# Performance work log

Measured on AMD Instinct MI355X. Metric: run time of the kernel, lower is better.

## Reference

```python
import jax, jax.numpy as jnp
import numpy as np

N, E = 100000, 1200000
IN_NF, H_NF, OUT_NF, IN_EF = 32, 64, 64, 16


def _linear_params(key, fan_in, fan_out):
    kw, kb = jax.random.split(key)
    s = 1.0 / np.sqrt(fan_in)
    W = jax.random.uniform(kw, (fan_in, fan_out), jnp.float32, -s, s)
    b = jax.random.uniform(kb, (fan_out,), jnp.float32, -s, s)
    return W, b


def setup_inputs() -> dict:
    key = jax.random.key(0)
    ks = jax.random.split(key, 16)
    inp = {
        'node_feats': jax.random.normal(ks[0], (N, IN_NF), jnp.float32),
        'edge_attr': jax.random.normal(ks[1], (E, IN_EF), jnp.float32),
        'coords': jax.random.normal(ks[2], (N, 3), jnp.float32),
        'edge_index': jax.random.randint(ks[3], (2, E), 0, N, jnp.int64),
    }
    # emb_in / emb_out
    inp['W_in'], inp['b_in'] = _linear_params(ks[4], IN_NF, H_NF)
    inp['W_out'], inp['b_out'] = _linear_params(ks[5], H_NF, OUT_NF)
    # edge MLP: cat[h_i, h_j, radial, edge_attr] -> hidden -> hidden
    edge_in = 2 * H_NF + 1 + IN_EF
    inp['We1'], inp['be1'] = _linear_params(ks[6], edge_in, H_NF)
    inp['We2'], inp['be2'] = _linear_params(ks[7], H_NF, H_NF)
    # node MLP: cat[h, agg_m] -> hidden -> out
    inp['Wn1'], inp['bn1'] = _linear_params(ks[8], H_NF + H_NF, H_NF)
    inp['Wn2'], inp['bn2'] = _linear_params(ks[9], H_NF, H_NF)
    # coord MLP: m -> hidden -> 1
    inp['Wc1'], inp['bc1'] = _linear_params(ks[10], H_NF, H_NF)
    inp['Wc2'], inp['bc2'] = _linear_params(ks[11], H_NF, 1)
    return inp


def _egnn_fwd(node_feats, edge_attr, coords, edge_index,
              W_in, b_in, We1, be1, We2, be2, Wn1, bn1, Wn2, bn2,
              Wc1, bc1, Wc2, bc2, W_out, b_out):
    relu = jax.nn.relu
    n = node_feats.shape[0]
    row, col = edge_index[0], edge_index[1]

    h = node_feats @ W_in + b_in                       # [N, H]

    # --- edge model ---
    coord_diff = coords[row] - coords[col]             # [E, 3]
    radial = jnp.sum(coord_diff * coord_diff, axis=-1, keepdims=True)  # [E, 1]
    edge_in = jnp.concatenate([h[row], h[col], radial, edge_attr], axis=-1)
    m = relu(relu(edge_in @ We1 + be1) @ We2 + be2)    # [E, H]

    # --- coord model: mean-aggregate coord_diff * phi_x(m) ---
    trans = coord_diff * (relu(m @ Wc1 + bc1) @ Wc2 + bc2)  # [E, 3]
    agg_x = jax.ops.segment_sum(trans, row, num_segments=n)
    cnt = jax.ops.segment_sum(jnp.ones((trans.shape[0],), trans.dtype), row, num_segments=n)
    coords = coords + agg_x / jnp.maximum(cnt, 1.0)[:, None]

    # --- node model: sum-aggregate messages ---
    agg_m = jax.ops.segment_sum(m, row, num_segments=n)  # [N, H]
    h = relu(jnp.concatenate([h, agg_m], axis=-1) @ Wn1 + bn1) @ Wn2 + bn2

    out = h @ W_out + b_out                            # [N, OUT]
    return out, coords


def reference(node_feats, edge_attr, coords, edge_index,
              W_in, b_in, W_out, b_out, We1, be1, We2, be2,
              Wn1, bn1, Wn2, bn2, Wc1, bc1, Wc2, bc2):
    return _egnn_fwd(node_feats, edge_attr, coords, edge_index,
                     W_in, b_in, We1, be1, We2, be2, Wn1, bn1, Wn2, bn2,
                     Wc1, bc1, Wc2, bc2, W_out, b_out)
```

## Files before the change

### kernel.cpp

```cpp
#include <hip/hip_runtime.h>


typedef __attribute__((ext_vector_type(4))) float f32x4;
typedef __attribute__((ext_vector_type(8))) short short8;

__device__ __forceinline__ void atomAddF(float* p, float v) { unsafeAtomicAdd(p, v); }

__device__ __forceinline__ unsigned short f2bf(float f) {
  unsigned int u = __builtin_bit_cast(unsigned int, f);
  unsigned int r = (u + 0x7FFFu + ((u >> 16) & 1u)) >> 16;
  return (unsigned short)r;
}
__device__ __forceinline__ float bf2f(unsigned short s) {
  unsigned int v = ((unsigned int)s) << 16;
  return __builtin_bit_cast(float, v);
}
__device__ __forceinline__ float lo_bf(unsigned int u) {
  return __builtin_bit_cast(float, u << 16);
}
__device__ __forceinline__ float hi_bf(unsigned int u) {
  return __builtin_bit_cast(float, u & 0xFFFF0000u);
}

__global__ __launch_bounds__(256) void k_prep(
    const float* __restrict__ nf, const float* __restrict__ W_in,
    const float* __restrict__ b_in, const float* __restrict__ We1,
    const float* __restrict__ be1, const float* __restrict__ Wn1,
    const float* __restrict__ bn1, const float* __restrict__ Wn2,
    const float* __restrict__ bn2, const float* __restrict__ W_out,
    const float* __restrict__ b_out, unsigned short* __restrict__ nfb,
    float* __restrict__ WA, float* __restrict__ WB, float* __restrict__ WF1,
    float* __restrict__ Wno, float* __restrict__ bSum, float* __restrict__ bn1f,
    float* __restrict__ bno, float* __restrict__ aggz, int N) {
  const int b = blockIdx.x, t = threadIdx.x;
  if (b == 0 || b == 1) {
    const float* Wsrc = (b == 0) ? We1 : (We1 + 64 * 64);
    float* dst = (b == 0) ? WA : WB;
    for (int idx = t; idx < 2048; idx += 256) {
      const int i = idx >> 6, n = idx & 63;
      float s = 0.f;
      for (int h = 0; h < 64; ++h) s = fmaf(W_in[i * 64 + h], Wsrc[h * 64 + n], s);
      dst[idx] = s;
    }
  } else if (b == 2) {
    for (int idx = t; idx < 2048; idx += 256) {
      const int i = idx >> 6, n = idx & 63;
      float s = 0.f;
      for (int h = 0; h < 64; ++h) s = fmaf(W_in[i * 64 + h], Wn1[h * 64 + n], s);
      WF1[idx] = s;
    }
    if (t < 64) {
      float s1 = bn1[t], s2 = be1[t];
      for (int h = 0; h < 64; ++h) {
        s1 = fmaf(b_in[h], Wn1[h * 64 + t], s1);
        s2 = fmaf(b_in[h], We1[h * 64 + t] + We1[(64 + h) * 64 + t], s2);
      }
      bn1f[t] = s1;
      bSum[t] = s2;
    }
  } else if (b <= 6) {
    const int base = (b - 3) * 1024;
    for (int idx = t; idx < 1024; idx += 256) {
      const int kk = (base + idx) >> 6, n = (base + idx) & 63;
      float s = 0.f;
      for (int h = 0; h < 64; ++h) s = fmaf(Wn2[kk * 64 + h], W_out[h * 64 + n], s);
      Wno[base + idx] = s;
    }
    if (b == 3 && t < 64) {
      float s = b_out[t];
      for (int h = 0; h < 64; ++h) s = fmaf(bn2[h], W_out[h * 64 + t], s);
      bno[t] = s;
    }
  } else {
    const int bid = b - 7, nb = gridDim.x - 7;
    const int tot8 = N * 8;
    for (int i = bid * 256 + t; i < tot8; i += nb * 256) {
      const f32x4 v = *reinterpret_cast<const f32x4*>(nf + (size_t)i * 4);
      ushort4 o;
      o.x = f2bf(v[0]); o.y = f2bf(v[1]); o.z = f2bf(v[2]); o.w = f2bf(v[3]);
      *reinterpret_cast<ushort4*>(nfb + (size_t)i * 4) = o;
    }
    const size_t tot = (size_t)N * 68;
    for (size_t i = (size_t)bid * 256 + t; i * 4 < tot; i += (size_t)nb * 256) {
      const size_t off = i * 4;
      if (off + 4 <= tot)
        *reinterpret_cast<float4*>(aggz + off) = make_float4(0.f, 0.f, 0.f, 0.f);
      else
        for (size_t q = off; q < tot; ++q) aggz[q] = 0.f;
    }
  }
}

__global__ __launch_bounds__(256) void k_gab(
    const float* __restrict__ nf, const float* __restrict__ WA,
    const float* __restrict__ WB, unsigned short* __restrict__ gA,
    unsigned short* __restrict__ gB, int N) {
  __shared__ float Ws[2 * 2048];
  __shared__ float nfl[4][8][36];
  for (int i = threadIdx.x; i < 2048; i += 256) {
    Ws[i] = WA[i];
    Ws[2048 + i] = WB[i];
  }
  __syncthreads();
  const int w = threadIdx.x >> 6, lane = threadIdx.x & 63;
  const int NG = (N + 7) >> 3;
  for (int ng = blockIdx.x * 4 + w; ng < NG; ng += gridDim.x * 4) {
    const int base = ng * 8;
    {
      const int nl = lane >> 3, ch = lane & 7;
      int n = base + nl;
      if (n >= N) n = N - 1;
      const f32x4 v = *reinterpret_cast<const f32x4*>(nf + (size_t)n * 32 + ch * 4);
      *reinterpret_cast<f32x4*>(&nfl[w][nl][ch * 4]) = v;
    }
    float aa[8], ab[8];
#pragma unroll
    for (int i = 0; i < 8; ++i) { aa[i] = 0.f; ab[i] = 0.f; }
    for (int k4 = 0; k4 < 8; ++k4) {
      float w0[2][4];
#pragma unroll
      for (int q = 0; q < 4; ++q) {
        w0[0][q] = Ws[(k4 * 4 + q) * 64 + lane];
        w0[1][q] = Ws[2048 + (k4 * 4 + q) * 64 + lane];
      }
#pragma unroll
      for (int i = 0; i < 8; ++i) {
        const f32x4 x = *reinterpret_cast<const f32x4*>(&nfl[w][i][k4 * 4]);
#pragma unroll
        for (int q = 0; q < 4; ++q) {
          aa[i] = fmaf(x[q], w0[0][q], aa[i]);
          ab[i] = fmaf(x[q], w0[1][q], ab[i]);
        }
      }
    }
#pragma unroll
    for (int i = 0; i < 8; ++i) {
      const int n = base + i;
      if (n < N) {
        gA[(size_t)n * 64 + lane] = f2bf(aa[i]);
        gB[(size_t)n * 64 + lane] = f2bf(ab[i]);
      }
    }
  }
}

__global__ __launch_bounds__(256) void k_hist(const int* __restrict__ eidx,
                                              int* __restrict__ deg, int E) {
  for (int e = blockIdx.x * 256 + threadIdx.x; e < E; e += gridDim.x * 256)
    atomicAdd(&deg[eidx[e]], 1);
}

__global__ __launch_bounds__(256) void k_scanA(const int* __restrict__ deg,
                                               int* __restrict__ excl,
                                               int* __restrict__ bsum, int N) {
  __shared__ int s[256];
  const int t = threadIdx.x;
  const int i = blockIdx.x * 256 + t;
  const int v = (i < N) ? deg[i] : 0;
  s[t] = v;
  __syncthreads();
#pragma unroll
  for (int off = 1; off < 256; off <<= 1) {
    int x = 0;
    if (t >= off) x = s[t - off];
    __syncthreads();
    s[t] += x;
    __syncthreads();
  }
  if (i < N) excl[i] = s[t] - v;
  if (t == 255) bsum[blockIdx.x] = s[255];
}

__global__ __launch_bounds__(256) void k_scanC(int* __restrict__ excl,
                                               const int* __restrict__ bsum,
                                               int N) {
  __shared__ int sh[256];
  const int t = threadIdx.x, b = blockIdx.x;
  int part = 0;
  for (int i = t; i < b; i += 256) part += bsum[i];
  sh[t] = part;
  __syncthreads();
#pragma unroll
  for (int off = 128; off; off >>= 1) {
    if (t < off) sh[t] += sh[t + off];
    __syncthreads();
  }
  const int add = sh[0];
  const int i = b * 256 + t;
  if (i < N) excl[i] += add;
}

__global__ __launch_bounds__(256) void k_scatter(
    const int* __restrict__ eidx, int* __restrict__ rowNext,
    unsigned long long* __restrict__ srt8, int E) {
  for (int e = blockIdx.x * 256 + threadIdx.x; e < E; e += gridDim.x * 256) {
    const int r = eidx[e];
    const int c = eidx[E + e];
    const int pos = atomicAdd(&rowNext[r], 1);
    srt8[pos] = (unsigned long long)r | ((unsigned long long)c << 18) |
                ((unsigned long long)e << 36);
  }
}

struct EdgeLds {
  unsigned short We2t[64 * 72];
  unsigned short Wc1t[64 * 72];
  unsigned short Bea[64 * 40];
  unsigned short x[4][32 * 72];
  float cd[4][32 * 4];
  int idx[4][32];
};

__global__ __launch_bounds__(256, 3) void k_edge(
    const unsigned short* __restrict__ gA, const unsigned short* __restrict__ gB,
    const float* __restrict__ ea, const float* __restrict__ co,
    const unsigned long long* __restrict__ srt8, const float* __restrict__ We1,
    const float* __restrict__ bSum, const float* __restrict__ be2,
    const float* __restrict__ We2, const float* __restrict__ bc1,
    const float* __restrict__ Wc1, const float* __restrict__ Wc2,
    const float* __restrict__ bc2, float* __restrict__ agg_m,
    float* __restrict__ agg_x, int E) {
  __shared__ EdgeLds S;
  const int tid = threadIdx.x;
  for (int i = tid; i < 4096; i += 256) {
    const int k = i >> 6, n = i & 63;
    S.We2t[n * 72 + k] = f2bf(We2[k * 64 + n]);
    S.Wc1t[n * 72 + k] = f2bf(Wc1[k * 64 + n]);
  }
  for (int i = tid; i < 2048; i += 256) {
    const int k = i >> 6, n = i & 63;
    const float v = (k < 16) ? We1[(129 + k) * 64 + n]
                             : ((k == 16) ? We1[128 * 64 + n] : 0.f);
    S.Bea[n * 40 + k] = f2bf(v);
  }
  __syncthreads();

  const int w = tid >> 6, lane = tid & 63;
  const int g = lane >> 4, t = lane & 15;
  const float bc2v = bc2[0];

  float bS_r[4], be2_r[4], bc1_r[4], wc2_r[4];
#pragma unroll
  for (int nt = 0; nt < 4; ++nt) {
    const int n = t + 16 * nt;
    bS_r[nt] = bSum[n];
    be2_r[nt] = be2[n];
    bc1_r[nt] = bc1[n];
    wc2_r[nt] = Wc2[n];
  }

  unsigned short* xw = &S.x[w][0];
  float* cdw = &S.cd[w][0];
  int* idxw = &S.idx[w][0];
  const int ngroups = (E + 31) >> 5;
  const int GS = gridDim.x * 4;

  int grp = blockIdx.x * 4 + w;
  unsigned long long s8 = 0;
  if (grp < ngroups && lane < 32) {
    int e = grp * 32 + lane;
    if (e >= E) e = E - 1;
    s8 = srt8[e];
  }

  for (; grp < ngroups; grp += GS) {
    const int e0 = grp * 32;
    unsigned long long s8n = 0;
    {
      const long gn = (long)grp + GS;
      if (lane < 32) {
        long e = gn * 32 + lane;
        if (e >= E) e = E - 1;
        s8n = srt8[e];
      }
    }
    const int r_dec = (int)(s8 & 0x3FFFFull);
    const int c_dec = (int)((s8 >> 18) & 0x3FFFFull);
    const int p_dec = (int)(s8 >> 36);
    if (lane < 32) idxw[lane] = r_dec;

    const int el0 = lane & 31;
    const int rE = __shfl(r_dec, el0, 64);
    const int cE = __shfl(c_dec, el0, 64);
    if (lane < 32) {
      const float dx = co[(size_t)rE * 3 + 0] - co[(size_t)cE * 3 + 0];
      const float dy = co[(size_t)rE * 3 + 1] - co[(size_t)cE * 3 + 1];
      const float dz = co[(size_t)rE * 3 + 2] - co[(size_t)cE * 3 + 2];
      f32x4 c4;
      c4[0] = dx; c4[1] = dy; c4[2] = dz; c4[3] = dx * dx + dy * dy + dz * dz;
      *reinterpret_cast<f32x4*>(&cdw[el0 * 4]) = c4;
    }

#pragma unroll
    for (int rr = 0; rr < 4; ++rr) {
      const int el = rr * 8 + (lane >> 3), ch = lane & 7;
      const int rI = __shfl(r_dec, el, 64);
      const int cI = __shfl(c_dec, el, 64);
      const uint4 va = *reinterpret_cast<const uint4*>(gA + (size_t)rI * 64 + ch * 8);
      const uint4 vb = *reinterpret_cast<const uint4*>(gB + (size_t)cI * 64 + ch * 8);
      const unsigned int a[4] = {va.x, va.y, va.z, va.w};
      const unsigned int b[4] = {vb.x, vb.y, vb.z, vb.w};
      uint4 o;
      unsigned int r[4];
#pragma unroll
      for (int q = 0; q < 4; ++q) {
        const float s0 = lo_bf(a[q]) + lo_bf(b[q]);
        const float s1 = hi_bf(a[q]) + hi_bf(b[q]);
        r[q] = ((unsigned int)f2bf(s1) << 16) | (unsigned int)f2bf(s0);
      }
      o.x = r[0]; o.y = r[1]; o.z = r[2]; o.w = r[3];
      *reinterpret_cast<uint4*>(&xw[el * 72 + ch * 8]) = o;
    }

    short8 a1[2];
#pragma unroll
    for (int mt = 0; mt < 2; ++mt) {
      const int eaI = __shfl(p_dec, t + 16 * mt, 64);
      short8 a = {};
      if (g < 2) {
        const float* pe2 = ea + (size_t)eaI * 16 + g * 8;
        const f32x4 x0 = *reinterpret_cast<const f32x4*>(pe2);
        const f32x4 x1 = *reinterpret_cast<const f32x4*>(pe2 + 4);
#pragma unroll
        for (int q = 0; q < 4; ++q) {
          a[q] = (short)f2bf(x0[q]);
          a[4 + q] = (short)f2bf(x1[q]);
        }
      } else if (g == 2) {
        a[0] = (short)f2bf(cdw[(t + 16 * mt) * 4 + 3]);
      }
      a1[mt] = a;
    }

    f32x4 acc[2][4];
#pragma unroll
    for (int mt = 0; mt < 2; ++mt)
#pragma unroll
      for (int nt = 0; nt < 4; ++nt)
#pragma unroll
        for (int j = 0; j < 4; ++j) {
          const int row = g * 4 + j + 16 * mt, col = t + 16 * nt;
          acc[mt][nt][j] = bf2f(xw[row * 72 + col]) + bS_r[nt];
        }
#pragma unroll
    for (int mt = 0; mt < 2; ++mt)
#pragma unroll
      for (int nt = 0; nt < 4; ++nt) {
        const short8 b = *reinterpret_cast<const short8*>(&S.Bea[(t + 16 * nt) * 40 + g * 8]);
        acc[mt][nt] = __builtin_amdgcn_mfma_f32_16x16x32_bf16(a1[mt], b, acc[mt][nt], 0, 0, 0);
      }
#pragma unroll
    for (int mt = 0; mt < 2; ++mt)
#pragma unroll
      for (int nt = 0; nt < 4; ++nt)
#pragma unroll
        for (int j = 0; j < 4; ++j) {
          const float v = fmaxf(acc[mt][nt][j], 0.f);
          xw[(g * 4 + j + 16 * mt) * 72 + t + 16 * nt] = f2bf(v);
        }
    short8 A2[2][2];
#pragma unroll
    for (int mt = 0; mt < 2; ++mt)
#pragma unroll
      for (int kt = 0; kt < 2; ++kt)
        A2[mt][kt] = *reinterpret_cast<const short8*>(&xw[(t + 16 * mt) * 72 + kt * 32 + g * 8]);
    f32x4 m2[2][4];
#pragma unroll
    for (int mt = 0; mt < 2; ++mt)
#pragma unroll
      for (int nt = 0; nt < 4; ++nt) {
        f32x4 c;
        c[0] = be2_r[nt]; c[1] = be2_r[nt]; c[2] = be2_r[nt]; c[3] = be2_r[nt];
#pragma unroll
        for (int kt = 0; kt < 2; ++kt) {
          const short8 b = *reinterpret_cast<const short8*>(
              &S.We2t[(t + 16 * nt) * 72 + kt * 32 + g * 8]);
          c = __builtin_amdgcn_mfma_f32_16x16x32_bf16(A2[mt][kt], b, c, 0, 0, 0);
        }
#pragma unroll
        for (int j = 0; j < 4; ++j) c[j] = fmaxf(c[j], 0.f);
        m2[mt][nt] = c;
      }
#pragma unroll
    for (int mt = 0; mt < 2; ++mt)
#pragma unroll
      for (int nt = 0; nt < 4; ++nt)
#pragma unroll
        for (int j = 0; j < 4; ++j)
          xw[(g * 4 + j + 16 * mt) * 72 + t + 16 * nt] = f2bf(m2[mt][nt][j]);

    short8 A3[2][2];
#pragma unroll
    for (int mt = 0; mt < 2; ++mt)
#pragma unroll
      for (int kt = 0; kt < 2; ++kt)
        A3[mt][kt] = *reinterpret_cast<const short8*>(&xw[(t + 16 * mt) * 72 + kt * 32 + g * 8]);
    float sv[2][4];
#pragma unroll
    for (int mt = 0; mt < 2; ++mt)
#pragma unroll
      for (int j = 0; j < 4; ++j) sv[mt][j] = 0.f;
#pragma unroll
    for (int mt = 0; mt < 2; ++mt)
#pragma unroll
      for (int nt = 0; nt < 4; ++nt) {
        f32x4 c;
        c[0] = bc1_r[nt]; c[1] = bc1_r[nt]; c[2] = bc1_r[nt]; c[3] = bc1_r[nt];
#pragma unroll
        for (int kt = 0; kt < 2; ++kt) {
          const short8 b = *reinterpret_cast<const short8*>(
              &S.Wc1t[(t + 16 * nt) * 72 + kt * 32 + g * 8]);
          c = __builtin_amdgcn_mfma_f32_16x16x32_bf16(A3[mt][kt], b, c, 0, 0, 0);
        }
#pragma unroll
        for (int j = 0; j < 4; ++j) sv[mt][j] = fmaf(fmaxf(c[j], 0.f), wc2_r[nt], sv[mt][j]);
      }
#pragma unroll
    for (int d = 1; d < 16; d <<= 1)
#pragma unroll
      for (int mt = 0; mt < 2; ++mt)
#pragma unroll
        for (int j = 0; j < 4; ++j) sv[mt][j] += __shfl_xor(sv[mt][j], d, 64);
#pragma unroll
    for (int mt = 0; mt < 2; ++mt)
#pragma unroll
      for (int j = 0; j < 4; ++j) sv[mt][j] += bc2v;

#pragma unroll
    for (int mt = 0; mt < 2; ++mt)
#pragma unroll
      for (int j = 0; j < 4; ++j)
        if (t == 0) cdw[(g * 4 + j + 16 * mt) * 4 + 3] = sv[mt][j];

    {
      float accm = 0.f;
#pragma unroll
      for (int r = 0; r < 32; ++r) {
        const int rIr = idxw[r];
        const bool valid = (e0 + r) < E;
        if (valid) accm += bf2f(xw[r * 72 + lane]);
        const bool closes = (r == 31) || ((e0 + r + 1) >= E) || (idxw[r + 1] != rIr);
        if (valid && closes) {
          atomAddF(&agg_m[(size_t)rIr * 64 + lane], accm);
          accm = 0.f;
        }
      }
    }
    if (lane < 3) {
      float accx = 0.f;
#pragma unroll
      for (int r = 0; r < 32; ++r) {
        const int rIr = idxw[r];
        const bool valid = (e0 + r) < E;
        if (valid) accx += cdw[r * 4 + lane] * cdw[r * 4 + 3];
        const bool closes = (r == 31) || ((e0 + r + 1) >= E) || (idxw[r + 1] != rIr);
        if (valid && closes) {
          atomAddF(&agg_x[(size_t)rIr * 3 + lane], accx);
          accx = 0.f;
        }
      }
    }
    s8 = s8n;
  }
}

struct NodeLds {
  unsigned short Wn1bT[64 * 72];
  unsigned short WnoT[64 * 72];
  unsigned short x[4][32 * 72];
};

__global__ __launch_bounds__(256, 4) void k_node(
    const unsigned short* __restrict__ nfb, const float* __restrict__ agg_m,
    const float* __restrict__ agg_x, const int* __restrict__ deg,
    const float* __restrict__ co, const float* __restrict__ WF1,
    const float* __restrict__ Wn1, const float* __restrict__ Wno,
    const float* __restrict__ bn1f, const float* __restrict__ bno,
    float* __restrict__ out, float* __restrict__ co_out, int N) {
  __shared__ NodeLds S;
  const int tid = threadIdx.x;
  for (int i = tid; i < 4096; i += 256) {
    const int k = i >> 6, n = i & 63;
    S.Wn1bT[n * 72 + k] = f2bf(Wn1[(64 + k) * 64 + n]);
    S.WnoT[n * 72 + k] = f2bf(Wno[k * 64 + n]);
  }
  __syncthreads();
  const int w = tid >> 6, lane = tid & 63;
  const int g = lane >> 4, t = lane & 15;

  short8 fW1[4];
  float b1_r[4], bo_r[4];
#pragma unroll
  for (int nt = 0; nt < 4; ++nt) {
    const int n = t + 16 * nt;
    short8 a;
#pragma unroll
    for (int j = 0; j < 8; ++j) a[j] = (short)f2bf(WF1[(g * 8 + j) * 64 + n]);
    fW1[nt] = a;
    b1_r[nt] = bn1f[n];
    bo_r[nt] = bno[n];
  }

  unsigned short* xw = &S.x[w][0];
  const int ngroups = (N + 31) >> 5;
  const int GS = gridDim.x * 4;

  for (int grp = blockIdx.x * 4 + w; grp < ngroups; grp += GS) {
    const int base = grp * 32;
    short8 A1[2], Aa[2][2];
#pragma unroll
    for (int mt = 0; mt < 2; ++mt) {
      int node = base + t + 16 * mt;
      if (node >= N) node = N - 1;
      A1[mt] = *reinterpret_cast<const short8*>(nfb + (size_t)node * 32 + g * 8);
#pragma unroll
      for (int kt = 0; kt < 2; ++kt) {
        const f32x4 v0 = *reinterpret_cast<const f32x4*>(
            agg_m + (size_t)node * 64 + kt * 32 + g * 8);
        const f32x4 v1 = *reinterpret_cast<const f32x4*>(
            agg_m + (size_t)node * 64 + kt * 32 + g * 8 + 4);
        short8 a;
#pragma unroll
        for (int j = 0; j < 4; ++j) {
          a[j] = (short)f2bf(v0[j]);
          a[4 + j] = (short)f2bf(v1[j]);
        }
        Aa[mt][kt] = a;
      }
    }
    f32x4 acc[2][4];
#pragma unroll
    for (int mt = 0; mt < 2; ++mt)
#pragma unroll
      for (int nt = 0; nt < 4; ++nt) {
        const int n = t + 16 * nt;
        f32x4 c;
        c[0] = b1_r[nt]; c[1] = b1_r[nt]; c[2] = b1_r[nt]; c[3] = b1_r[nt];
        c = __builtin_amdgcn_mfma_f32_16x16x32_bf16(A1[mt], fW1[nt], c, 0, 0, 0);
#pragma unroll
        for (int kt = 0; kt < 2; ++kt) {
          const short8 b = *reinterpret_cast<const short8*>(
              &S.Wn1bT[n * 72 + kt * 32 + g * 8]);
          c = __builtin_amdgcn_mfma_f32_16x16x32_bf16(Aa[mt][kt], b, c, 0, 0, 0);
        }
        acc[mt][nt] = c;
      }
#pragma unroll
    for (int mt = 0; mt < 2; ++mt)
#pragma unroll
      for (int nt = 0; nt < 4; ++nt)
#pragma unroll
        for (int j = 0; j < 4; ++j)
          xw[(g * 4 + j + 16 * mt) * 72 + t + 16 * nt] =
              f2bf(fmaxf(acc[mt][nt][j], 0.f));
    short8 A2[2][2];
#pragma unroll
    for (int mt = 0; mt < 2; ++mt)
#pragma unroll
      for (int kt = 0; kt < 2; ++kt)
        A2[mt][kt] = *reinterpret_cast<const short8*>(
            &S.x[w][(t + 16 * mt) * 72 + kt * 32 + g * 8]);
#pragma unroll
    for (int mt = 0; mt < 2; ++mt)
#pragma unroll
      for (int nt = 0; nt < 4; ++nt) {
        const int n = t + 16 * nt;
        f32x4 c;
        c[0] = bo_r[nt]; c[1] = bo_r[nt]; c[2] = bo_r[nt]; c[3] = bo_r[nt];
#pragma unroll
        for (int kt = 0; kt < 2; ++kt) {
          const short8 b = *reinterpret_cast<const short8*>(
              &S.WnoT[n * 72 + kt * 32 + g * 8]);
          c = __builtin_amdgcn_mfma_f32_16x16x32_bf16(A2[mt][kt], b, c, 0, 0, 0);
        }
#pragma unroll
        for (int j = 0; j < 4; ++j) {
          const int node = base + g * 4 + j + 16 * mt;
          if (node < N) out[(size_t)node * 64 + n] = c[j];
        }
      }
    if (lane < 32) {
      const int node = base + lane;
      if (node < N) {
        const float dv = fmaxf((float)deg[node], 1.f);
#pragma unroll
        for (int d = 0; d < 3; ++d)
          co_out[(size_t)node * 3 + d] =
              co[(size_t)node * 3 + d] + agg_x[(size_t)node * 3 + d] / dv;
      }
    }
  }
}

extern "C" void kernel_launch(void* const* d_in, const int* in_sizes, int n_in,
                              void* d_out, int out_size, void* d_ws, size_t ws_size,
                              hipStream_t stream) {
  const float* nf = (const float*)d_in[0];
  const float* ea = (const float*)d_in[1];
  const float* co = (const float*)d_in[2];
  const int* ei = (const int*)d_in[3];
  const float* W_in = (const float*)d_in[4];
  const float* b_in = (const float*)d_in[5];
  const float* W_out = (const float*)d_in[6];
  const float* b_out = (const float*)d_in[7];
  const float* We1 = (const float*)d_in[8];
  const float* be1 = (const float*)d_in[9];
  const float* We2 = (const float*)d_in[10];
  const float* be2 = (const float*)d_in[11];
  const float* Wn1 = (const float*)d_in[12];
  const float* bn1 = (const float*)d_in[13];
  const float* Wn2 = (const float*)d_in[14];
  const float* bn2 = (const float*)d_in[15];
  const float* Wc1 = (const float*)d_in[16];
  const float* bc1 = (const float*)d_in[17];
  const float* Wc2 = (const float*)d_in[18];
  const float* bc2 = (const float*)d_in[19];

  const int N = in_sizes[0] / 32;
  const int E = in_sizes[1] / 16;

  float* ws = (float*)d_ws;
  float* agg_m = ws;
  float* agg_x = agg_m + (size_t)N * 64;
  int* deg = (int*)(agg_x + (size_t)N * 3);
  float* WA = (float*)(deg + N);
  float* WB = WA + 2048;
  float* WF1 = WB + 2048;
  float* Wno = WF1 + 2048;
  float* bSum = Wno + 4096;
  float* bn1f = bSum + 64;
  float* bno = bn1f + 64;
  int* rowNext = (int*)(bno + 64);
  int* bsumBuf = rowNext + N;
  uintptr_t pp = (uintptr_t)(bsumBuf + 512);
  pp = (pp + 7) & ~(uintptr_t)7;
  unsigned long long* srt8 = (unsigned long long*)pp;
  unsigned short* nfb = (unsigned short*)(srt8 + E);

  float* outp = (float*)d_out;
  float* co_out = outp + (size_t)N * 64;
  unsigned short* gA = (unsigned short*)d_out;
  unsigned short* gB = gA + (size_t)N * 64;

  const int nb = (N + 255) / 256;

  k_prep<<<1031, 256, 0, stream>>>(nf, W_in, b_in, We1, be1, Wn1, bn1, Wn2,
                                   bn2, W_out, b_out, nfb, WA, WB, WF1, Wno,
                                   bSum, bn1f, bno, agg_m, N);
  k_gab<<<2048, 256, 0, stream>>>(nf, WA, WB, gA, gB, N);
  k_hist<<<512, 256, 0, stream>>>(ei, deg, E);
  k_scanA<<<nb, 256, 0, stream>>>(deg, rowNext, bsumBuf, N);
  k_scanC<<<nb, 256, 0, stream>>>(rowNext, bsumBuf, N);
  k_scatter<<<512, 256, 0, stream>>>(ei, rowNext, srt8, E);
  k_edge<<<768, 256, 0, stream>>>(gA, gB, ea, co, srt8, We1, bSum, be2, We2,
                                  bc1, Wc1, Wc2, bc2, agg_m, agg_x, E);
  k_node<<<1024, 256, 0, stream>>>(nfb, agg_m, agg_x, deg, co, WF1, Wn1, Wno,
                                   bn1f, bno, outp, co_out, N);
}
```

Measured before the change: 434.8 us.

## Read transposed bf16 MLP weights from global memory instead of LDS in edge kernel

Precomputes transposed bf16 copies of We2 and Wc1 once in the prep kernel and has the edge kernel load MFMA B-operands directly from global (cache-resident) memory rather than staging them into shared memory per block. This removes the per-block LDS fill and shrinks LDS usage, which allows more resident blocks, and the edge grid is doubled to use that occupancy. An opaque zero offset keeps the compiler from hoisting the weight loads out of the loop, so they are re-read through the cache on every iteration. That adds global/L1 traffic in exchange.

```diff
diff --git a/kernel.cpp b/kernel.cpp
--- a/kernel.cpp
+++ b/kernel.cpp
@@ -25,13 +25,15 @@
 __global__ __launch_bounds__(256) void k_prep(
     const float* __restrict__ nf, const float* __restrict__ W_in,
     const float* __restrict__ b_in, const float* __restrict__ We1,
-    const float* __restrict__ be1, const float* __restrict__ Wn1,
+    const float* __restrict__ be1, const float* __restrict__ We2,
+    const float* __restrict__ Wc1, const float* __restrict__ Wn1,
     const float* __restrict__ bn1, const float* __restrict__ Wn2,
     const float* __restrict__ bn2, const float* __restrict__ W_out,
     const float* __restrict__ b_out, unsigned short* __restrict__ nfb,
     float* __restrict__ WA, float* __restrict__ WB, float* __restrict__ WF1,
     float* __restrict__ Wno, float* __restrict__ bSum, float* __restrict__ bn1f,
-    float* __restrict__ bno, float* __restrict__ aggz, int N) {
+    float* __restrict__ bno, unsigned short* __restrict__ wt2g,
+    unsigned short* __restrict__ wtc1g, float* __restrict__ aggz, int N) {
   const int b = blockIdx.x, t = threadIdx.x;
   if (b == 0 || b == 1) {
     const float* Wsrc = (b == 0) ? We1 : (We1 + 64 * 64);
@@ -71,8 +73,14 @@
       for (int h = 0; h < 64; ++h) s = fmaf(bn2[h], W_out[h * 64 + t], s);
       bno[t] = s;
     }
+  } else if (b == 7) {
+    for (int i = t; i < 4096; i += 256) {
+      const int k = i >> 6, n = i & 63;
+      wt2g[n * 64 + k] = f2bf(We2[k * 64 + n]);
+      wtc1g[n * 64 + k] = f2bf(Wc1[k * 64 + n]);
+    }
   } else {
-    const int bid = b - 7, nb = gridDim.x - 7;
+    const int bid = b - 8, nb = gridDim.x - 8;
     const int tot8 = N * 8;
     for (int i = bid * 256 + t; i < tot8; i += nb * 256) {
       const f32x4 v = *reinterpret_cast<const f32x4*>(nf + (size_t)i * 4);
@@ -203,8 +211,6 @@
 }
 
 struct EdgeLds {
-  unsigned short We2t[64 * 72];
-  unsigned short Wc1t[64 * 72];
   unsigned short Bea[64 * 40];
   unsigned short x[4][32 * 72];
   float cd[4][32 * 4];
@@ -216,17 +222,12 @@
     const float* __restrict__ ea, const float* __restrict__ co,
     const unsigned long long* __restrict__ srt8, const float* __restrict__ We1,
     const float* __restrict__ bSum, const float* __restrict__ be2,
-    const float* __restrict__ We2, const float* __restrict__ bc1,
-    const float* __restrict__ Wc1, const float* __restrict__ Wc2,
+    const unsigned short* __restrict__ wt2g, const float* __restrict__ bc1,
+    const unsigned short* __restrict__ wtc1g, const float* __restrict__ Wc2,
     const float* __restrict__ bc2, float* __restrict__ agg_m,
     float* __restrict__ agg_x, int E) {
   __shared__ EdgeLds S;
   const int tid = threadIdx.x;
-  for (int i = tid; i < 4096; i += 256) {
-    const int k = i >> 6, n = i & 63;
-    S.We2t[n * 72 + k] = f2bf(We2[k * 64 + n]);
-    S.Wc1t[n * 72 + k] = f2bf(Wc1[k * 64 + n]);
-  }
   for (int i = tid; i < 2048; i += 256) {
     const int k = i >> 6, n = i & 63;
     const float v = (k < 16) ? We1[(129 + k) * 64 + n]
@@ -265,6 +266,11 @@
 
   for (; grp < ngroups; grp += GS) {
     const int e0 = grp * 32;
+    int zofs = 0;
+    asm volatile("" : "+v"(zofs));
+    const unsigned short* wt2p = wt2g + zofs;
+    const unsigned short* wc1p = wtc1g + zofs;
+
     unsigned long long s8n = 0;
     {
       const long gn = (long)grp + GS;
@@ -374,7 +380,7 @@
 #pragma unroll
         for (int kt = 0; kt < 2; ++kt) {
           const short8 b = *reinterpret_cast<const short8*>(
-              &S.We2t[(t + 16 * nt) * 72 + kt * 32 + g * 8]);
+              wt2p + (size_t)(t + 16 * nt) * 64 + kt * 32 + g * 8);
           c = __builtin_amdgcn_mfma_f32_16x16x32_bf16(A2[mt][kt], b, c, 0, 0, 0);
         }
 #pragma unroll
@@ -409,7 +415,7 @@
 #pragma unroll
         for (int kt = 0; kt < 2; ++kt) {
           const short8 b = *reinterpret_cast<const short8*>(
-              &S.Wc1t[(t + 16 * nt) * 72 + kt * 32 + g * 8]);
+              wc1p + (size_t)(t + 16 * nt) * 64 + kt * 32 + g * 8);
           c = __builtin_amdgcn_mfma_f32_16x16x32_bf16(A3[mt][kt], b, c, 0, 0, 0);
         }
 #pragma unroll
@@ -636,6 +642,8 @@
   pp = (pp + 7) & ~(uintptr_t)7;
   unsigned long long* srt8 = (unsigned long long*)pp;
   unsigned short* nfb = (unsigned short*)(srt8 + E);
+  unsigned short* wt2g = nfb + (size_t)N * 32;
+  unsigned short* wtc1g = wt2g + 4096;
 
   float* outp = (float*)d_out;
   float* co_out = outp + (size_t)N * 64;
@@ -644,16 +652,17 @@
 
   const int nb = (N + 255) / 256;
 
-  k_prep<<<1031, 256, 0, stream>>>(nf, W_in, b_in, We1, be1, Wn1, bn1, Wn2,
-                                   bn2, W_out, b_out, nfb, WA, WB, WF1, Wno,
-                                   bSum, bn1f, bno, agg_m, N);
+  k_prep<<<1032, 256, 0, stream>>>(nf, W_in, b_in, We1, be1, We2, Wc1, Wn1,
+                                   bn1, Wn2, bn2, W_out, b_out, nfb, WA, WB,
+                                   WF1, Wno, bSum, bn1f, bno, wt2g, wtc1g,
+                                   agg_m, N);
   k_gab<<<2048, 256, 0, stream>>>(nf, WA, WB, gA, gB, N);
   k_hist<<<512, 256, 0, stream>>>(ei, deg, E);
   k_scanA<<<nb, 256, 0, stream>>>(deg, rowNext, bsumBuf, N);
   k_scanC<<<nb, 256, 0, stream>>>(rowNext, bsumBuf, N);
   k_scatter<<<512, 256, 0, stream>>>(ei, rowNext, srt8, E);
-  k_edge<<<768, 256, 0, stream>>>(gA, gB, ea, co, srt8, We1, bSum, be2, We2,
-                                  bc1, Wc1, Wc2, bc2, agg_m, agg_x, E);
+  k_edge<<<1536, 256, 0, stream>>>(gA, gB, ea, co, srt8, We1, bSum, be2, wt2g,
+                                   bc1, wtc1g, Wc2, bc2, agg_m, agg_x, E);
   k_node<<<1024, 256, 0, stream>>>(nfb, agg_m, agg_x, deg, co, WF1, Wn1, Wno,
                                    bn1f, bno, outp, co_out, N);
 }
```

New measurement: 449.4 us. 1.03x slower.
